# Optimization experiments

Measured on AMD Instinct MI355X. Metric: run time of the kernel, lower is better.

The kernel has to match this reference:

```python
import jax, jax.numpy as jnp
import numpy as np

B, L, D, H, FF, K = 2, 2048, 512, 16, 2048, 5
HD = D // H
EPS = 1e-5


def _ln(x, g, b):
    m = jnp.mean(x, axis=-1, keepdims=True)
    v = jnp.var(x, axis=-1, keepdims=True)
    return (x - m) / jnp.sqrt(v + EPS) * g + b


def _rope_table(seq_len, hd):
    pos = jnp.arange(seq_len, dtype=jnp.float32)
    inv = 1.0 / (10000.0 ** (jnp.arange(0, hd, 2, dtype=jnp.float32) / hd))
    ang = pos[:, None] * inv[None, :]            # [L, hd/2]
    return jnp.concatenate([jnp.cos(ang), jnp.sin(ang)], axis=-1)  # [L, hd]


def setup_inputs() -> dict:
    key = jax.random.key(0)
    ks = jax.random.split(key, 32)
    w = lambda k, shape: jax.random.normal(k, shape, jnp.float32) * 0.02
    z = lambda n: jnp.zeros((n,), jnp.float32)
    o = lambda n: jnp.ones((n,), jnp.float32)
    return {
        'src': jax.random.normal(ks[0], (B, L, D), jnp.float32),
        'Wq': w(ks[1], (D, D)), 'bq': z(D),
        'Wk': w(ks[2], (D, D)), 'bk': z(D),
        'Wv': w(ks[3], (D, D)), 'bv': z(D),
        'Wo': w(ks[4], (D, D)), 'bo': z(D),
        'ln_g': o(D), 'ln_b': z(D),
        'pw1_w': w(ks[5], (2 * D, D)), 'pw1_b': z(2 * D),
        'dw_w': w(ks[6], (D, 1, K)), 'dw_b': z(D),
        'bn_g': o(D), 'bn_b': z(D),
        'pw2_w': w(ks[7], (D, D)), 'pw2_b': z(D),
        'proj_w': w(ks[8], (L, L)), 'proj_b': z(L),
        'proj2_w': w(ks[9], (D, D)), 'proj2_b': z(D),
        'W1': w(ks[10], (FF, D)), 'b1': z(FF),
        'W2': w(ks[11], (D, FF)), 'b2': z(D),
        'n1_g': o(D), 'n1_b': z(D),
        'n2_g': o(D), 'n2_b': z(D),
    }


def reference(src, Wq, bq, Wk, bk, Wv, bv, Wo, bo, ln_g, ln_b,
              pw1_w, pw1_b, dw_w, dw_b, bn_g, bn_b, pw2_w, pw2_b,
              proj_w, proj_b, proj2_w, proj2_b, W1, b1, W2, b2,
              n1_g, n1_b, n2_g, n2_b):
    scale = HD ** -0.5
    pe = _rope_table(L, HD)
    c, s = pe[:, ::2], pe[:, 1::2]   # faithful to apply_RoPE's interleaved slicing of [cos|sin]

    def rope(x):  # x: [B,H,L,hd]
        xe, xo = x[..., ::2], x[..., 1::2]
        return jnp.concatenate([xe * c - xo * s, xe * s + xo * c], axis=-1)

    q = (src @ Wq.T + bq).reshape(B, L, H, HD).transpose(0, 2, 1, 3)
    k = (src @ Wk.T + bk).reshape(B, L, H, HD).transpose(0, 2, 1, 3)
    v = (src @ Wv.T + bv).reshape(B, L, H, HD).transpose(0, 2, 1, 3)
    q, k = rope(q), rope(k)

    slopes = jnp.asarray(2.0 ** (-(2.0 ** (-(np.log2(H) - 3.0))) * np.arange(H)), jnp.float32)
    idx = jnp.arange(L)
    dist = jnp.clip(idx[:, None] - idx[None, :], 0, None).astype(jnp.float32)
    alibi = slopes[:, None, None] * dist  # [H,L,L]

    scores = jnp.einsum('bhld,bhmd->bhlm', q, k) * scale + alibi[None]
    attn = jax.nn.softmax(scores, axis=-1)
    ctx = jnp.einsum('bhlm,bhmd->bhld', attn, v).transpose(0, 2, 1, 3).reshape(B, L, D)
    attn_out = ctx @ Wo.T + bo

    x0 = src + _ln(attn_out, n1_g, n1_b)

    # depthwise conformer conv block (stride=1, residual downsample = identity)
    x = _ln(x0, ln_g, ln_b)
    x = x @ pw1_w.T + pw1_b                      # [B,L,2D]
    a, g = x[..., :D], x[..., D:]
    x = a * jax.nn.sigmoid(g)                    # GLU
    x = x.transpose(0, 2, 1)                     # [B,D,L]
    x = jax.lax.conv_general_dilated(x, dw_w, (1,), [(K // 2, K // 2)],
                                     dimension_numbers=('NCH', 'OIH', 'NCH'),
                                     feature_group_count=D) + dw_b[None, :, None]
    x = x * (bn_g / jnp.sqrt(1.0 + EPS))[None, :, None] + bn_b[None, :, None]  # BN eval (mu=0, var=1)
    x = x * jnp.clip(x + 3.0, 0.0, 6.0) / 6.0    # hardswish
    conv = x.transpose(0, 2, 1) @ pw2_w.T + pw2_b + x0

    # seq-dim projection branch
    p = jnp.einsum('bld,ml->bmd', x0, proj_w) + proj_b[None, :, None]
    p = p @ proj2_w.T + proj2_b

    y = p + conv
    ff = jax.nn.gelu(y @ W1.T + b1, approximate=False) @ W2.T + b2
    return _ln(y + ff, n2_g, n2_b)
```

## Files before the change

kernel.cpp:

```cpp
#include <hip/hip_runtime.h>
#include <math.h>

#define B_ 2
#define L_ 2048
#define D_ 512
#define H_ 16
#define HD_ 32
#define FF_ 2048
#define BL_ 4096
#define EPS_ 1e-5f

typedef unsigned short ushort;
typedef unsigned int uint;
typedef __attribute__((ext_vector_type(8))) short bf16x8;
typedef __attribute__((ext_vector_type(4))) float f32x4;
typedef __attribute__((ext_vector_type(4))) uint u32x4;

__device__ __forceinline__ ushort bf16r(float f) {
  uint u = __float_as_uint(f);
  uint r = (u + 0x7FFFu + ((u >> 16) & 1u)) >> 16;
  return (ushort)r;
}
__device__ __forceinline__ float bf2f(uint u) { return __uint_as_float(u << 16); }

__device__ __forceinline__ float wsum(float v) {
#pragma unroll
  for (int o = 32; o; o >>= 1) v += __shfl_xor(v, o);
  return v;
}

__device__ __forceinline__ void gload16(const void* g, void* l) {
  __builtin_amdgcn_global_load_lds(
      (const __attribute__((address_space(1))) void*)g,
      (__attribute__((address_space(3))) void*)l, 16, 0, 0);
}

template <int TMv, int TNv, int EPI, int BROW, int GELU, int RES, int OUTF, int OUTB>
__global__ __launch_bounds__(256, 2) void gemm_bf_k(
    const ushort* __restrict__ A, const ushort* __restrict__ W,
    const float* __restrict__ bias, const float* __restrict__ res,
    float* __restrict__ Cf, ushort* __restrict__ Cb,
    const int M, const int N, const int Kd, const long sW, const long sC,
    const int ldC,
    const float* __restrict__ tab, ushort* __restrict__ Qb,
    ushort* __restrict__ Kb, ushort* __restrict__ Vb) {
  constexpr int MF = (TMv == 128) ? 4 : ((TNv == 128) ? 4 : 2);
  constexpr int NF = (TNv == 128) ? ((TMv == 128) ? 4 : 2) : 2;
  __shared__ __align__(16) ushort As[TMv * 64];
  __shared__ __align__(16) ushort Ws[TNv * 64];
  const int tid = threadIdx.x;
  const int wid = tid >> 6, lane = tid & 63;
  const int lane15 = lane & 15, lgrp = lane >> 4;
  const int rowoff = (TMv == 128) ? (wid >> 1) * 64
                                  : ((TNv == 64) ? (wid >> 1) * 32 : 0);
  const int wnoff = (TMv == 128) ? (wid & 1) * 64
                                 : ((TNv == 128) ? wid * 32 : (wid & 1) * 32);
  const int bm = blockIdx.y * TMv, bn = blockIdx.x * TNv;
  const int z = blockIdx.z;
  const ushort* Wz = W + (size_t)z * sW;

  f32x4 acc[MF][NF];
#pragma unroll
  for (int i = 0; i < MF; ++i)
#pragma unroll
    for (int j = 0; j < NF; ++j) acc[i][j] = (f32x4){0.f, 0.f, 0.f, 0.f};

  for (int k0 = 0; k0 < Kd; k0 += 64) {
    __syncthreads();
#pragma unroll
    for (int i = 0; i < TMv / 32; ++i) {
      const int cb = i * 256 + wid * 64;
      const int chunk = cb + lane;
      const int ml = chunk >> 3;
      const int c16 = (chunk & 7) ^ (ml & 7);
      gload16(A + (size_t)(bm + ml) * Kd + k0 + c16 * 8, &As[(size_t)cb * 8]);
    }
#pragma unroll
    for (int i = 0; i < TNv / 32; ++i) {
      const int cb = i * 256 + wid * 64;
      const int chunk = cb + lane;
      const int ml = chunk >> 3;
      const int c16 = (chunk & 7) ^ (ml & 7);
      gload16(Wz + (size_t)(bn + ml) * Kd + k0 + c16 * 8, &Ws[(size_t)cb * 8]);
    }
    __syncthreads();

    bf16x8 af[2][MF], wf[2][NF];
#pragma unroll
    for (int kk = 0; kk < 2; ++kk) {
#pragma unroll
      for (int f = 0; f < MF; ++f) {
        const int ma = rowoff + f * 16 + lane15;
        const int ca = (kk * 4 + lgrp) ^ (ma & 7);
        af[kk][f] = *(const bf16x8*)&As[ma * 64 + ca * 8];
      }
#pragma unroll
      for (int f = 0; f < NF; ++f) {
        const int nb = wnoff + f * 16 + lane15;
        const int cw = (kk * 4 + lgrp) ^ (nb & 7);
        wf[kk][f] = *(const bf16x8*)&Ws[nb * 64 + cw * 8];
      }
    }
#pragma unroll
    for (int kk = 0; kk < 2; ++kk)
#pragma unroll
      for (int fm = 0; fm < MF; ++fm)
#pragma unroll
        for (int fn = 0; fn < NF; ++fn)
          acc[fm][fn] = __builtin_amdgcn_mfma_f32_16x16x32_bf16(
              af[kk][fm], wf[kk][fn], acc[fm][fn], 0, 0, 0);
  }

#pragma unroll
  for (int fm = 0; fm < MF; ++fm) {
#pragma unroll
    for (int fn = 0; fn < NF; ++fn) {
      const int n = bn + wnoff + fn * 16 + lane15;
      float bcol = 0.f;
      if (EPI == 2) bcol = bias[(n >> 1) + (n & 1) * 512];
      else if (EPI == 1 || !BROW) bcol = bias[n];
#pragma unroll
      for (int r = 0; r < 4; ++r) {
        const int m = bm + rowoff + fm * 16 + lgrp * 4 + r;
        float val = acc[fm][fn][r];
        if (EPI == 1) {
          val += bcol;
          float p = __shfl_xor(val, 1);
          const int l = m & 2047, b = m >> 11;
          const int h = (n >> 5) & 15;
          if (n < 1024) {
            const int ch = n & 31, i2 = ch >> 1;
            const float cv = tab[l * 32 + i2], sv = tab[l * 32 + 16 + i2];
            const float o = (ch & 1) ? (p * sv + val * cv) : (val * cv - p * sv);
            const int dcol = (ch & 1) ? 16 + i2 : i2;
            if (n < 512)
              Qb[(((size_t)(b * 16 + h)) * 2048 + l) * 32 + dcol] =
                  bf16r(o * (0.1767766952966369f * 1.4426950408889634f));
            else
              Kb[(((size_t)(b * 16 + h)) * 2048 + l) * 32 + dcol] = bf16r(o);
          } else {
            Vb[(((size_t)(b * 16 + h)) * 2048 + l) * 32 + (n & 31)] = bf16r(val);
          }
        } else if (EPI == 2) {
          val += bcol;
          float p = __shfl_xor(val, 1);
          if (!(n & 1)) {
            float glu = val / (1.f + __expf(-p));
            Cb[(size_t)m * 512 + (n >> 1)] = bf16r(glu);
          }
        } else {
          val += BROW ? bias[m] : bcol;
          if (RES) val += res[(size_t)m * N + n];
          if (GELU) val = 0.5f * val * (1.f + erff(val * 0.70710678118654752f));
          const size_t o = (size_t)z * sC + (size_t)m * ldC + n;
          if (OUTF) Cf[o] = val;
          if (OUTB) Cb[o] = bf16r(val);
        }
      }
    }
  }
}

struct CvtArgs {
  const float* s[11];
  ushort* d[11];
  int n[11];
  int pm[11];
};
__global__ __launch_bounds__(256) void cvt_all_k(CvtArgs a) {
  const int seg = blockIdx.y;
  const int n = a.n[seg];
  const int i = (blockIdx.x * 256 + threadIdx.x) * 8;
  if (i >= n) return;
  const float* s = a.s[seg] + i;
  float4 x = *(const float4*)s, y = *(const float4*)(s + 4);
  bf16x8 o;
  o[0] = (short)bf16r(x.x); o[1] = (short)bf16r(x.y);
  o[2] = (short)bf16r(x.z); o[3] = (short)bf16r(x.w);
  o[4] = (short)bf16r(y.x); o[5] = (short)bf16r(y.y);
  o[6] = (short)bf16r(y.z); o[7] = (short)bf16r(y.w);
  ushort* d = a.d[seg] + i;
  const int pm = a.pm[seg];
  if (pm == 1) {
    int cc = i >> 3;
    int row = cc >> 6, off = cc & 63;
    int nrow = (row < 512) ? row * 2 : (row - 512) * 2 + 1;
    d = a.d[seg] + (((size_t)nrow << 6) + off) * 8;
  } else if (pm >= 2) {
    d = a.d[seg] + (size_t)(i >> 9) * 1024 + (i & 511) + ((pm == 3) ? 512 : 0);
  }
  *(bf16x8*)d = o;
}

__global__ void misc_k(float* __restrict__ tab, const float* __restrict__ bq,
                       const float* __restrict__ bk, const float* __restrict__ bv,
                       float* __restrict__ bqkv, const float* __restrict__ p2b,
                       const float* __restrict__ pw2b, float* __restrict__ bcat) {
  if (blockIdx.x < 128) {
    int t = blockIdx.x * 256 + threadIdx.x;
    int i = t & 15, l = t >> 4;
    float cv, sv;
    if (i < 8) {
      float inv0 = 1.0f / powf(10000.0f, (float)(2 * i) / 16.0f);
      float inv1 = 1.0f / powf(10000.0f, (float)(2 * i + 1) / 16.0f);
      cv = cosf((float)l * inv0);
      sv = cosf((float)l * inv1);
    } else {
      int ii = i - 8;
      float inv0 = 1.0f / powf(10000.0f, (float)(2 * ii) / 16.0f);
      float inv1 = 1.0f / powf(10000.0f, (float)(2 * ii + 1) / 16.0f);
      cv = sinf((float)l * inv0);
      sv = sinf((float)l * inv1);
    }
    tab[l * 32 + i] = cv;
    tab[l * 32 + 16 + i] = sv;
  } else {
    int i = threadIdx.x;
    bqkv[i] = bq[i];            bqkv[i + 256] = bq[i + 256];
    bqkv[512 + i] = bk[i];      bqkv[768 + i] = bk[i + 256];
    bqkv[1024 + i] = bv[i];     bqkv[1280 + i] = bv[i + 256];
    bcat[i] = p2b[i] + pw2b[i];
    bcat[i + 256] = p2b[i + 256] + pw2b[i + 256];
  }
}

__global__ __launch_bounds__(256) void transp_k(const float* __restrict__ x,
                                                ushort* __restrict__ xT) {
  __shared__ float t[32][33];
  const int b = blockIdx.z, l0 = blockIdx.x * 32, d0 = blockIdx.y * 32;
  const int tx = threadIdx.x & 31, ty = threadIdx.x >> 5;
#pragma unroll
  for (int i = 0; i < 4; ++i)
    t[ty + i * 8][tx] = x[((size_t)(b * L_ + l0 + ty + i * 8)) * D_ + d0 + tx];
  __syncthreads();
#pragma unroll
  for (int i = 0; i < 4; ++i)
    xT[((size_t)(b * D_ + d0 + ty + i * 8)) * L_ + l0 + tx] =
        bf16r(t[tx][ty + i * 8]);
}

__global__ __launch_bounds__(256, 4) void attn_mfma_k(const ushort* __restrict__ q,
                                                      const ushort* __restrict__ k,
                                                      const ushort* __restrict__ v,
                                                      ushort* __restrict__ ctx) {
  __shared__ __align__(16) ushort K_lds[4][130][8];
  __shared__ __align__(16) uint V_lds[32][68];
  const int tid = threadIdx.x;
  const int wid = tid >> 6, lane = tid & 63;
  const int s = lane >> 4, lr = lane & 15;
  const int bid = blockIdx.x;
  const int xcd = bid & 7, idx = bid >> 3;
  const int bh = xcd * 4 + (idx & 3);
  const int qt = idx >> 2;
  const int qb = qt * 64;
  const int h = bh & 15, bidx = bh >> 4;
  const float nslope = -exp2f(-0.5f * (float)h) * 1.4426950408889634f;
  const int qrow = qb + wid * 16 + lr;
  const float qgf = (float)qrow;
  const float cq = nslope * qgf;
  bf16x8 qa = *(const bf16x8*)&q[((size_t)bh * L_ + qrow) * HD_ + s * 8];

  float lsum = 0.f;
  f32x4 acc0 = {0.f, 0.f, 0.f, 0.f}, acc1 = {0.f, 0.f, 0.f, 0.f};
  const ushort* kg = k + (size_t)bh * L_ * HD_;
  const ushort* vg = v + (size_t)bh * L_ * HD_;
  const int vslot = (lane & 48) + ((lane >> 1) & 3) * 4 + ((lane >> 3) & 1) * 2 + (lane & 1);

  for (int t0 = 0; t0 < L_; t0 += 128) {
    __syncthreads();
#pragma unroll
    for (int pass = 0; pass < 2; ++pass) {
      int id = tid + pass * 256;
      int key = id >> 2, slot = id & 3;
      *(bf16x8*)&K_lds[slot][key][0] =
          *(const bf16x8*)&kg[(size_t)(t0 + key) * HD_ + slot * 8];
    }
    {
      const ushort* g0 = vg + (size_t)(t0 + 2 * lane) * HD_ + wid * 8;
      u32x4 va = *(const u32x4*)g0;
      u32x4 vb = *(const u32x4*)(g0 + HD_);
#pragma unroll
      for (int w = 0; w < 4; ++w) {
        V_lds[wid * 8 + 2 * w][vslot] =
            __builtin_amdgcn_perm(vb[w], va[w], 0x05040100u);
        V_lds[wid * 8 + 2 * w + 1][vslot] =
            __builtin_amdgcn_perm(vb[w], va[w], 0x07060302u);
      }
    }
    __syncthreads();

    f32x4 sc[8];
    __builtin_amdgcn_s_setprio(1);
#pragma unroll
    for (int c = 0; c < 8; ++c) {
      bf16x8 kf = *(const bf16x8*)&K_lds[s][c * 16 + lr][0];
      f32x4 zz = {0.f, 0.f, 0.f, 0.f};
      sc[c] = __builtin_amdgcn_mfma_f32_16x16x32_bf16(kf, qa, zz, 0, 0, 0);
    }
    __builtin_amdgcn_s_setprio(0);
    if (t0 + 128 <= qb) {
      const float kb0 = (float)(t0 + s * 4);
#pragma unroll
      for (int c = 0; c < 8; ++c) {
        const float kc = kb0 + (float)(c * 16);
#pragma unroll
        for (int r = 0; r < 4; ++r) {
          float p = exp2f(fmaf(nslope, kc + (float)r, sc[c][r]));
          sc[c][r] = p;
          lsum += p;
        }
      }
    } else if (t0 >= qb + 64) {
#pragma unroll
      for (int c = 0; c < 8; ++c)
#pragma unroll
        for (int r = 0; r < 4; ++r) {
          float p = exp2f(sc[c][r] + cq);
          sc[c][r] = p;
          lsum += p;
        }
    } else {
      const float kb0 = (float)(t0 + s * 4);
#pragma unroll
      for (int c = 0; c < 8; ++c) {
        const float kc = kb0 + (float)(c * 16);
#pragma unroll
        for (int r = 0; r < 4; ++r) {
          float kpos = kc + (float)r;
          float mn = fminf(kpos, qgf);
          float p = exp2f(fmaf(nslope, mn, sc[c][r]));
          sc[c][r] = p;
          lsum += p;
        }
      }
    }
#pragma unroll
    for (int t = 0; t < 4; ++t) {
      uint w0 = __builtin_amdgcn_perm(__float_as_uint(sc[2 * t][1]),
                                      __float_as_uint(sc[2 * t][0]), 0x07060302u);
      uint w1 = __builtin_amdgcn_perm(__float_as_uint(sc[2 * t][3]),
                                      __float_as_uint(sc[2 * t][2]), 0x07060302u);
      uint w2 = __builtin_amdgcn_perm(__float_as_uint(sc[2 * t + 1][1]),
                                      __float_as_uint(sc[2 * t + 1][0]), 0x07060302u);
      uint w3 = __builtin_amdgcn_perm(__float_as_uint(sc[2 * t + 1][3]),
                                      __float_as_uint(sc[2 * t + 1][2]), 0x07060302u);
      u32x4 pw = {w0, w1, w2, w3};
      bf16x8 pf = __builtin_bit_cast(bf16x8, pw);
      bf16x8 v0 = *(const bf16x8*)&V_lds[lr][t * 16 + s * 4];
      bf16x8 v1 = *(const bf16x8*)&V_lds[16 + lr][t * 16 + s * 4];
      __builtin_amdgcn_s_setprio(1);
      acc0 = __builtin_amdgcn_mfma_f32_16x16x32_bf16(pf, v0, acc0, 0, 0, 0);
      acc1 = __builtin_amdgcn_mfma_f32_16x16x32_bf16(pf, v1, acc1, 0, 0, 0);
      __builtin_amdgcn_s_setprio(0);
    }
  }
  lsum += __shfl_xor(lsum, 16);
  lsum += __shfl_xor(lsum, 32);
#pragma unroll
  for (int r = 0; r < 4; ++r) {
    float ls = __shfl(lsum, s * 4 + r, 64);
    float il = 1.f / ls;
    int qg2 = qb + wid * 16 + s * 4 + r;
    ushort* op = ctx + ((size_t)(bidx * L_ + qg2)) * D_ + h * HD_;
    op[lr] = bf16r(acc0[r] * il);
    op[16 + lr] = bf16r(acc1[r] * il);
  }
}

__global__ __launch_bounds__(64) void ln_res_ln_k(
    const float* __restrict__ x, const float* __restrict__ res,
    const float* __restrict__ g1, const float* __restrict__ b1,
    const float* __restrict__ g2, const float* __restrict__ b2,
    float* __restrict__ x0, ushort* __restrict__ xln) {
  int row = blockIdx.x, lane = threadIdx.x;
  const float* xr = x + (size_t)row * D_;
  float v[8];
  float s = 0.f, ss = 0.f;
#pragma unroll
  for (int i = 0; i < 8; ++i) {
    float t = xr[i * 64 + lane];
    v[i] = t; s += t; ss += t * t;
  }
  s = wsum(s); ss = wsum(ss);
  float mean = s * (1.f / 512.f);
  float rstd = rsqrtf(ss * (1.f / 512.f) - mean * mean + EPS_);
  float w[8];
  float s2 = 0.f, ss2 = 0.f;
#pragma unroll
  for (int i = 0; i < 8; ++i) {
    int idx = i * 64 + lane;
    float t = res[(size_t)row * D_ + idx] + (v[i] - mean) * rstd * g1[idx] + b1[idx];
    w[i] = t; s2 += t; ss2 += t * t;
  }
  s2 = wsum(s2); ss2 = wsum(ss2);
  float mean2 = s2 * (1.f / 512.f);
  float rstd2 = rsqrtf(ss2 * (1.f / 512.f) - mean2 * mean2 + EPS_);
#pragma unroll
  for (int i = 0; i < 8; ++i) {
    int idx = i * 64 + lane;
    x0[(size_t)row * D_ + idx] = w[i];
    xln[(size_t)row * D_ + idx] = bf16r((w[i] - mean2) * rstd2 * g2[idx] + b2[idx]);
  }
}

__global__ __launch_bounds__(64) void ln_k(const float* __restrict__ x,
                                           const float* __restrict__ g,
                                           const float* __restrict__ bb,
                                           float* __restrict__ out) {
  int row = blockIdx.x, lane = threadIdx.x;
  const float* xr = x + (size_t)row * D_;
  float v[8];
  float s = 0.f, ss = 0.f;
#pragma unroll
  for (int i = 0; i < 8; ++i) {
    float t = xr[i * 64 + lane];
    v[i] = t; s += t; ss += t * t;
  }
  s = wsum(s); ss = wsum(ss);
  float mean = s * (1.f / 512.f);
  float rstd = rsqrtf(ss * (1.f / 512.f) - mean * mean + EPS_);
#pragma unroll
  for (int i = 0; i < 8; ++i) {
    int idx = i * 64 + lane;
    out[(size_t)row * D_ + idx] = (v[i] - mean) * rstd * g[idx] + bb[idx];
  }
}

__global__ __launch_bounds__(256) void convbn_k(
    const ushort* __restrict__ x, const float* __restrict__ w,
    const float* __restrict__ wb, const float* __restrict__ bng,
    const float* __restrict__ bnb, ushort* __restrict__ out) {
  int t = blockIdx.x * 256 + threadIdx.x;
  int c4 = t & 127;
  int l = (t >> 7) & 2047;
  int b = t >> 18;
  int d0 = c4 * 4;
  float accv[4] = {0.f, 0.f, 0.f, 0.f};
#pragma unroll
  for (int kt = 0; kt < 5; ++kt) {
    int ls = l + kt - 2;
    if (ls >= 0 && ls < L_) {
      uint2 xv = *(const uint2*)&x[((size_t)(b * L_ + ls)) * D_ + d0];
      float pv[4] = {bf2f(xv.x & 0xffffu), bf2f(xv.x >> 16),
                     bf2f(xv.y & 0xffffu), bf2f(xv.y >> 16)};
#pragma unroll
      for (int j = 0; j < 4; ++j) accv[j] += pv[j] * w[(d0 + j) * 5 + kt];
    }
  }
  const float bscale = rsqrtf(1.0f + EPS_);
  float po[4];
#pragma unroll
  for (int j = 0; j < 4; ++j) {
    int d = d0 + j;
    float vv = accv[j] + wb[d];
    vv = vv * (bng[d] * bscale) + bnb[d];
    float hs = fminf(fmaxf(vv + 3.f, 0.f), 6.f);
    po[j] = vv * hs * (1.f / 6.f);
  }
  uint lo = (uint)bf16r(po[0]) | ((uint)bf16r(po[1]) << 16);
  uint hi = (uint)bf16r(po[2]) | ((uint)bf16r(po[3]) << 16);
  uint2 o2 = {lo, hi};
  *(uint2*)&out[((size_t)(b * L_ + l)) * 1024 + d0] = o2;
}

extern "C" void kernel_launch(void* const* d_in, const int* in_sizes, int n_in,
                              void* d_out, int out_size, void* d_ws, size_t ws_size,
                              hipStream_t stream) {
  const float* src    = (const float*)d_in[0];
  const float* Wq     = (const float*)d_in[1];
  const float* bq     = (const float*)d_in[2];
  const float* Wk     = (const float*)d_in[3];
  const float* bk     = (const float*)d_in[4];
  const float* Wv     = (const float*)d_in[5];
  const float* bv     = (const float*)d_in[6];
  const float* Wo     = (const float*)d_in[7];
  const float* bo     = (const float*)d_in[8];
  const float* ln_g   = (const float*)d_in[9];
  const float* ln_b   = (const float*)d_in[10];
  const float* pw1_w  = (const float*)d_in[11];
  const float* pw1_b  = (const float*)d_in[12];
  const float* dw_w   = (const float*)d_in[13];
  const float* dw_b   = (const float*)d_in[14];
  const float* bn_g   = (const float*)d_in[15];
  const float* bn_b   = (const float*)d_in[16];
  const float* pw2_w  = (const float*)d_in[17];
  const float* pw2_b  = (const float*)d_in[18];
  const float* proj_w = (const float*)d_in[19];
  const float* proj_b = (const float*)d_in[20];
  const float* proj2_w= (const float*)d_in[21];
  const float* proj2_b= (const float*)d_in[22];
  const float* W1     = (const float*)d_in[23];
  const float* b1     = (const float*)d_in[24];
  const float* W2     = (const float*)d_in[25];
  const float* b2     = (const float*)d_in[26];
  const float* n1_g   = (const float*)d_in[27];
  const float* n1_b   = (const float*)d_in[28];
  const float* n2_g   = (const float*)d_in[29];
  const float* n2_b   = (const float*)d_in[30];
  float* out = (float*)d_out;

  char* wsb = (char*)d_ws;
  const size_t MB1 = 1 << 20;
  ushort* wqkv = (ushort*)(wsb);
  ushort* wo_w = (ushort*)(wsb + 1536 * 1024);
  ushort* pw1w = (ushort*)(wsb + 2 * MB1);
  ushort* wcat = (ushort*)(wsb + 3 * MB1);
  ushort* pjww = (ushort*)(wsb + 4 * MB1);
  ushort* w1w  = (ushort*)(wsb + 12 * MB1);
  ushort* w2w  = (ushort*)(wsb + 14 * MB1);
  float*  bqkv = (float*)(wsb + 16 * MB1);
  float*  bcat = (float*)(wsb + 16 * MB1 + 6144);
  float*  tab  = (float*)(wsb + 16 * MB1 + 8192);
  char* A0 = wsb + 17 * MB1;
  ushort* src_bf = (ushort*)A0;
  ushort* ff_bf  = (ushort*)A0;
  float*  x0     = (float*)(A0 + 8 * MB1);
  char* B0 = A0 + 16 * MB1;
  ushort* Qb = (ushort*)B0;
  ushort* Kb = (ushort*)(B0 + 4 * MB1);
  ushort* Vb = (ushort*)(B0 + 8 * MB1);
  ushort* glu_bf = (ushort*)B0;
  ushort* xln_bf = (ushort*)(B0 + 8 * MB1);
  ushort* cat_bf = (ushort*)(B0 + 4 * MB1);
  float*  zbuf   = (float*)B0;
  char* C0 = B0 + 12 * MB1;
  ushort* ctx_bf = (ushort*)C0;
  ushort* x0T    = (ushort*)C0;
  ushort* y_bf   = (ushort*)C0;
  char* D0 = C0 + 4 * MB1;
  float* attnout = (float*)D0;
  float* y       = (float*)D0;

  dim3 blk(256);

  CvtArgs ca;
  for (int i = 0; i < 11; ++i) ca.pm[i] = 0;
  ca.s[0] = Wq;     ca.d[0] = wqkv;              ca.n[0] = 512 * 512;
  ca.s[1] = Wk;     ca.d[1] = wqkv + 512 * 512;  ca.n[1] = 512 * 512;
  ca.s[2] = Wv;     ca.d[2] = wqkv + 1024 * 512; ca.n[2] = 512 * 512;
  ca.s[3] = Wo;     ca.d[3] = wo_w;              ca.n[3] = 512 * 512;
  ca.s[4] = pw1_w;  ca.d[4] = pw1w;              ca.n[4] = 1024 * 512; ca.pm[4] = 1;
  ca.s[5] = pw2_w;  ca.d[5] = wcat;              ca.n[5] = 512 * 512;  ca.pm[5] = 3;
  ca.s[6] = proj_w; ca.d[6] = pjww;              ca.n[6] = 2048 * 2048;
  ca.s[7] = proj2_w;ca.d[7] = wcat;              ca.n[7] = 512 * 512;  ca.pm[7] = 2;
  ca.s[8] = W1;     ca.d[8] = w1w;               ca.n[8] = 2048 * 512;
  ca.s[9] = W2;     ca.d[9] = w2w;               ca.n[9] = 512 * 2048;
  ca.s[10]= src;    ca.d[10]= src_bf;            ca.n[10]= BL_ * D_;
  cvt_all_k<<<dim3(2048, 11), blk, 0, stream>>>(ca);
  misc_k<<<dim3(129), blk, 0, stream>>>(tab, bq, bk, bv, bqkv, proj2_b, pw2_b, bcat);

  gemm_bf_k<64,128,1,0,0,0,0,0><<<dim3(12, 64), blk, 0, stream>>>(
      src_bf, wqkv, bqkv, nullptr, nullptr, nullptr,
      BL_, 1536, 512, 0, 0, 1536, tab, Qb, Kb, Vb);

  attn_mfma_k<<<dim3(1024), blk, 0, stream>>>(Qb, Kb, Vb, ctx_bf);

  gemm_bf_k<64,64,0,0,0,0,1,0><<<dim3(8, 64), blk, 0, stream>>>(
      ctx_bf, wo_w, bo, nullptr, attnout, nullptr,
      BL_, 512, 512, 0, 0, 512, nullptr, nullptr, nullptr, nullptr);

  ln_res_ln_k<<<BL_, 64, 0, stream>>>(attnout, src, n1_g, n1_b, ln_g, ln_b,
                                      x0, xln_bf);

  transp_k<<<dim3(64, 16, 2), blk, 0, stream>>>(x0, x0T);

  gemm_bf_k<64,128,2,0,0,0,0,1><<<dim3(8, 64), blk, 0, stream>>>(
      xln_bf, pw1w, pw1_b, nullptr, nullptr, glu_bf,
      BL_, 1024, 512, 0, 0, 512, nullptr, nullptr, nullptr, nullptr);

  convbn_k<<<(B_ * L_ * (D_ / 4)) / 256, blk, 0, stream>>>(
      glu_bf, dw_w, dw_b, bn_g, bn_b, cat_bf + 512);

  gemm_bf_k<64,64,0,1,0,0,0,1><<<dim3(8, 32, 2), blk, 0, stream>>>(
      pjww, x0T, proj_b, nullptr, nullptr, cat_bf,
      2048, 512, 2048, (long)512 * 2048, (long)2048 * 1024, 1024,
      nullptr, nullptr, nullptr, nullptr);

  gemm_bf_k<64,64,0,0,0,1,1,1><<<dim3(8, 64), blk, 0, stream>>>(
      cat_bf, wcat, bcat, x0, y, y_bf,
      BL_, 512, 1024, 0, 0, 512, nullptr, nullptr, nullptr, nullptr);

  gemm_bf_k<128,128,0,0,1,0,0,1><<<dim3(16, 32), blk, 0, stream>>>(
      y_bf, w1w, b1, nullptr, nullptr, ff_bf,
      BL_, 2048, 512, 0, 0, 2048, nullptr, nullptr, nullptr, nullptr);

  gemm_bf_k<64,64,0,0,0,1,1,0><<<dim3(8, 64), blk, 0, stream>>>(
      ff_bf, w2w, b2, y, zbuf, nullptr,
      BL_, 512, 2048, 0, 0, 512, nullptr, nullptr, nullptr, nullptr);

  ln_k<<<BL_, 64, 0, stream>>>(zbuf, n2_g, n2_b, out);
}
```

Baseline: 241.4 us.

## Widen attention blocks to 128 queries and compute softmax denominator via MFMA

Attention blocks become 512 threads covering 128 query rows, which halves the grid and the number of times each K/V tile is staged into LDS per query. The per-lane K/V load work shrinks to match. The softmax row sum moves from scalar adds plus cross-lane shuffles to an extra MFMA against a vector of ones. That adds one MFMA per tile but removes the VALU accumulation. Larger blocks may lower occupancy, and the denominator is now built from bf16-rounded probabilities.

Measured after the change: 241.0 us. About the same (-0.2%).

```diff
diff --git a/kernel.cpp b/kernel.cpp
--- a/kernel.cpp
+++ b/kernel.cpp
@@ -239,7 +239,7 @@
         bf16r(t[tx][ty + i * 8]);
 }
 
-__global__ __launch_bounds__(256, 4) void attn_mfma_k(const ushort* __restrict__ q,
+__global__ __launch_bounds__(512, 4) void attn_mfma_k(const ushort* __restrict__ q,
                                                       const ushort* __restrict__ k,
                                                       const ushort* __restrict__ v,
                                                       ushort* __restrict__ ctx) {
@@ -252,7 +252,7 @@
   const int xcd = bid & 7, idx = bid >> 3;
   const int bh = xcd * 4 + (idx & 3);
   const int qt = idx >> 2;
-  const int qb = qt * 64;
+  const int qb = qt * 128;
   const int h = bh & 15, bidx = bh >> 4;
   const float nslope = -exp2f(-0.5f * (float)h) * 1.4426950408889634f;
   const int qrow = qb + wid * 16 + lr;
@@ -260,32 +260,31 @@
   const float cq = nslope * qgf;
   bf16x8 qa = *(const bf16x8*)&q[((size_t)bh * L_ + qrow) * HD_ + s * 8];
 
-  float lsum = 0.f;
+  bf16x8 vones;
+#pragma unroll
+  for (int i = 0; i < 8; ++i) vones[i] = (short)0x3F80;
+
   f32x4 acc0 = {0.f, 0.f, 0.f, 0.f}, acc1 = {0.f, 0.f, 0.f, 0.f};
+  f32x4 accl = {0.f, 0.f, 0.f, 0.f};
   const ushort* kg = k + (size_t)bh * L_ * HD_;
   const ushort* vg = v + (size_t)bh * L_ * HD_;
   const int vslot = (lane & 48) + ((lane >> 1) & 3) * 4 + ((lane >> 3) & 1) * 2 + (lane & 1);
 
   for (int t0 = 0; t0 < L_; t0 += 128) {
     __syncthreads();
-#pragma unroll
-    for (int pass = 0; pass < 2; ++pass) {
-      int id = tid + pass * 256;
-      int key = id >> 2, slot = id & 3;
+    {
+      int key = tid >> 2, slot = tid & 3;
       *(bf16x8*)&K_lds[slot][key][0] =
           *(const bf16x8*)&kg[(size_t)(t0 + key) * HD_ + slot * 8];
     }
     {
-      const ushort* g0 = vg + (size_t)(t0 + 2 * lane) * HD_ + wid * 8;
-      u32x4 va = *(const u32x4*)g0;
-      u32x4 vb = *(const u32x4*)(g0 + HD_);
-#pragma unroll
-      for (int w = 0; w < 4; ++w) {
-        V_lds[wid * 8 + 2 * w][vslot] =
-            __builtin_amdgcn_perm(vb[w], va[w], 0x05040100u);
-        V_lds[wid * 8 + 2 * w + 1][vslot] =
-            __builtin_amdgcn_perm(vb[w], va[w], 0x07060302u);
-      }
+      const ushort* g0 = vg + (size_t)(t0 + 2 * lane) * HD_ + wid * 4;
+      uint2 va = *(const uint2*)g0;
+      uint2 vb = *(const uint2*)(g0 + HD_);
+      V_lds[wid * 4 + 0][vslot] = __builtin_amdgcn_perm(vb.x, va.x, 0x05040100u);
+      V_lds[wid * 4 + 1][vslot] = __builtin_amdgcn_perm(vb.x, va.x, 0x07060302u);
+      V_lds[wid * 4 + 2][vslot] = __builtin_amdgcn_perm(vb.y, va.y, 0x05040100u);
+      V_lds[wid * 4 + 3][vslot] = __builtin_amdgcn_perm(vb.y, va.y, 0x07060302u);
     }
     __syncthreads();
 
@@ -298,27 +297,20 @@
       sc[c] = __builtin_amdgcn_mfma_f32_16x16x32_bf16(kf, qa, zz, 0, 0, 0);
     }
     __builtin_amdgcn_s_setprio(0);
-    if (t0 + 128 <= qb) {
+    if (t0 < qb) {
       const float kb0 = (float)(t0 + s * 4);
 #pragma unroll
       for (int c = 0; c < 8; ++c) {
         const float kc = kb0 + (float)(c * 16);
 #pragma unroll
-        for (int r = 0; r < 4; ++r) {
-          float p = exp2f(fmaf(nslope, kc + (float)r, sc[c][r]));
-          sc[c][r] = p;
-          lsum += p;
-        }
+        for (int r = 0; r < 4; ++r)
+          sc[c][r] = exp2f(fmaf(nslope, kc + (float)r, sc[c][r]));
       }
-    } else if (t0 >= qb + 64) {
+    } else if (t0 > qb) {
 #pragma unroll
       for (int c = 0; c < 8; ++c)
 #pragma unroll
-        for (int r = 0; r < 4; ++r) {
-          float p = exp2f(sc[c][r] + cq);
-          sc[c][r] = p;
-          lsum += p;
-        }
+        for (int r = 0; r < 4; ++r) sc[c][r] = exp2f(sc[c][r] + cq);
     } else {
       const float kb0 = (float)(t0 + s * 4);
 #pragma unroll
@@ -326,11 +318,8 @@
         const float kc = kb0 + (float)(c * 16);
 #pragma unroll
         for (int r = 0; r < 4; ++r) {
-          float kpos = kc + (float)r;
-          float mn = fminf(kpos, qgf);
-          float p = exp2f(fmaf(nslope, mn, sc[c][r]));
-          sc[c][r] = p;
-          lsum += p;
+          float mn = fminf(kc + (float)r, qgf);
+          sc[c][r] = exp2f(fmaf(nslope, mn, sc[c][r]));
         }
       }
     }
@@ -351,15 +340,13 @@
       __builtin_amdgcn_s_setprio(1);
       acc0 = __builtin_amdgcn_mfma_f32_16x16x32_bf16(pf, v0, acc0, 0, 0, 0);
       acc1 = __builtin_amdgcn_mfma_f32_16x16x32_bf16(pf, v1, acc1, 0, 0, 0);
+      accl = __builtin_amdgcn_mfma_f32_16x16x32_bf16(pf, vones, accl, 0, 0, 0);
       __builtin_amdgcn_s_setprio(0);
     }
   }
-  lsum += __shfl_xor(lsum, 16);
-  lsum += __shfl_xor(lsum, 32);
 #pragma unroll
   for (int r = 0; r < 4; ++r) {
-    float ls = __shfl(lsum, s * 4 + r, 64);
-    float il = 1.f / ls;
+    float il = 1.f / accl[r];
     int qg2 = qb + wid * 16 + s * 4 + r;
     ushort* op = ctx + ((size_t)(bidx * L_ + qg2)) * D_ + h * HD_;
     op[lr] = bf16r(acc0[r] * il);
@@ -553,7 +540,7 @@
       src_bf, wqkv, bqkv, nullptr, nullptr, nullptr,
       BL_, 1536, 512, 0, 0, 1536, tab, Qb, Kb, Vb);
 
-  attn_mfma_k<<<dim3(1024), blk, 0, stream>>>(Qb, Kb, Vb, ctx_bf);
+  attn_mfma_k<<<dim3(512), dim3(512), 0, stream>>>(Qb, Kb, Vb, ctx_bf);
 
   gemm_bf_k<64,64,0,0,0,0,1,0><<<dim3(8, 64), blk, 0, stream>>>(
       ctx_bf, wo_w, bo, nullptr, attnout, nullptr,
```

## Double-buffer GEMM LDS tiles and process two query tiles per attention wave

Applied to the files above, without the earlier changes.

The GEMM kernel now double-buffers its A and W tiles in LDS. It issues the next k-tile's global-to-LDS loads before computing the current one, syncing with explicit vmcnt waits and barriers. The attention kernel now has each wave handle 32 query rows, sharing each K/V LDS tile across twice the work, and the grid is halved. The softmax denominator moves from a scalar sum plus shuffles to an extra MFMA against a vector of ones. The cost is doubled LDS in the GEMM and more registers in attention, which may reduce occupancy, and the denominator is now built from bf16-rounded probabilities.

Result: slower. 319.7 us (+32.4%).

```diff
diff --git a/kernel.cpp b/kernel.cpp
--- a/kernel.cpp
+++ b/kernel.cpp
@@ -46,8 +46,9 @@
     ushort* __restrict__ Kb, ushort* __restrict__ Vb) {
   constexpr int MF = (TMv == 128) ? 4 : ((TNv == 128) ? 4 : 2);
   constexpr int NF = (TNv == 128) ? ((TMv == 128) ? 4 : 2) : 2;
-  __shared__ __align__(16) ushort As[TMv * 64];
-  __shared__ __align__(16) ushort Ws[TNv * 64];
+  constexpr int NLD = TMv / 32 + TNv / 32;
+  __shared__ __align__(16) ushort As[2][TMv * 64];
+  __shared__ __align__(16) ushort Ws[2][TNv * 64];
   const int tid = threadIdx.x;
   const int wid = tid >> 6, lane = tid & 63;
   const int lane15 = lane & 15, lgrp = lane >> 4;
@@ -58,22 +59,16 @@
   const int bm = blockIdx.y * TMv, bn = blockIdx.x * TNv;
   const int z = blockIdx.z;
   const ushort* Wz = W + (size_t)z * sW;
-
-  f32x4 acc[MF][NF];
-#pragma unroll
-  for (int i = 0; i < MF; ++i)
-#pragma unroll
-    for (int j = 0; j < NF; ++j) acc[i][j] = (f32x4){0.f, 0.f, 0.f, 0.f};
-
-  for (int k0 = 0; k0 < Kd; k0 += 64) {
-    __syncthreads();
+  const int NT = Kd >> 6;
+
+  auto STAGE = [&](ushort* dA, ushort* dW, int k0) {
 #pragma unroll
     for (int i = 0; i < TMv / 32; ++i) {
       const int cb = i * 256 + wid * 64;
       const int chunk = cb + lane;
       const int ml = chunk >> 3;
       const int c16 = (chunk & 7) ^ (ml & 7);
-      gload16(A + (size_t)(bm + ml) * Kd + k0 + c16 * 8, &As[(size_t)cb * 8]);
+      gload16(A + (size_t)(bm + ml) * Kd + k0 + c16 * 8, dA + (size_t)cb * 8);
     }
 #pragma unroll
     for (int i = 0; i < TNv / 32; ++i) {
@@ -81,9 +76,29 @@
       const int chunk = cb + lane;
       const int ml = chunk >> 3;
       const int c16 = (chunk & 7) ^ (ml & 7);
-      gload16(Wz + (size_t)(bn + ml) * Kd + k0 + c16 * 8, &Ws[(size_t)cb * 8]);
-    }
-    __syncthreads();
+      gload16(Wz + (size_t)(bn + ml) * Kd + k0 + c16 * 8, dW + (size_t)cb * 8);
+    }
+  };
+
+  f32x4 acc[MF][NF];
+#pragma unroll
+  for (int i = 0; i < MF; ++i)
+#pragma unroll
+    for (int j = 0; j < NF; ++j) acc[i][j] = (f32x4){0.f, 0.f, 0.f, 0.f};
+
+  STAGE(&As[0][0], &Ws[0][0], 0);
+
+  int cur = 0;
+  for (int t = 0; t < NT; ++t) {
+    const int nxt = cur ^ 1;
+    if (t + 1 < NT) {
+      STAGE(&As[nxt][0], &Ws[nxt][0], (t + 1) << 6);
+      asm volatile("s_waitcnt vmcnt(%0)" ::"n"(NLD) : "memory");
+    } else {
+      asm volatile("s_waitcnt vmcnt(0)" ::: "memory");
+    }
+    __builtin_amdgcn_s_barrier();
+    __builtin_amdgcn_sched_barrier(0);
 
     bf16x8 af[2][MF], wf[2][NF];
 #pragma unroll
@@ -92,13 +107,13 @@
       for (int f = 0; f < MF; ++f) {
         const int ma = rowoff + f * 16 + lane15;
         const int ca = (kk * 4 + lgrp) ^ (ma & 7);
-        af[kk][f] = *(const bf16x8*)&As[ma * 64 + ca * 8];
+        af[kk][f] = *(const bf16x8*)&As[cur][ma * 64 + ca * 8];
       }
 #pragma unroll
       for (int f = 0; f < NF; ++f) {
         const int nb = wnoff + f * 16 + lane15;
         const int cw = (kk * 4 + lgrp) ^ (nb & 7);
-        wf[kk][f] = *(const bf16x8*)&Ws[nb * 64 + cw * 8];
+        wf[kk][f] = *(const bf16x8*)&Ws[cur][nb * 64 + cw * 8];
       }
     }
 #pragma unroll
@@ -109,6 +124,10 @@
         for (int fn = 0; fn < NF; ++fn)
           acc[fm][fn] = __builtin_amdgcn_mfma_f32_16x16x32_bf16(
               af[kk][fm], wf[kk][fn], acc[fm][fn], 0, 0, 0);
+
+    asm volatile("" ::: "memory");
+    __builtin_amdgcn_s_barrier();
+    cur = nxt;
   }
 
 #pragma unroll
@@ -252,16 +271,23 @@
   const int xcd = bid & 7, idx = bid >> 3;
   const int bh = xcd * 4 + (idx & 3);
   const int qt = idx >> 2;
-  const int qb = qt * 64;
+  const int qb = qt * 128;
   const int h = bh & 15, bidx = bh >> 4;
   const float nslope = -exp2f(-0.5f * (float)h) * 1.4426950408889634f;
-  const int qrow = qb + wid * 16 + lr;
-  const float qgf = (float)qrow;
-  const float cq = nslope * qgf;
-  bf16x8 qa = *(const bf16x8*)&q[((size_t)bh * L_ + qrow) * HD_ + s * 8];
-
-  float lsum = 0.f;
-  f32x4 acc0 = {0.f, 0.f, 0.f, 0.f}, acc1 = {0.f, 0.f, 0.f, 0.f};
+  const int qrowA = qb + wid * 32 + lr;
+  const int qrowB = qrowA + 16;
+  const float qgfA = (float)qrowA, qgfB = (float)qrowB;
+  const float cqA = nslope * qgfA, cqB = nslope * qgfB;
+  bf16x8 qa0 = *(const bf16x8*)&q[((size_t)bh * L_ + qrowA) * HD_ + s * 8];
+  bf16x8 qa1 = *(const bf16x8*)&q[((size_t)bh * L_ + qrowB) * HD_ + s * 8];
+
+  bf16x8 vones;
+#pragma unroll
+  for (int i = 0; i < 8; ++i) vones[i] = (short)0x3F80;
+
+  f32x4 accA0 = {0.f, 0.f, 0.f, 0.f}, accA1 = {0.f, 0.f, 0.f, 0.f};
+  f32x4 accB0 = {0.f, 0.f, 0.f, 0.f}, accB1 = {0.f, 0.f, 0.f, 0.f};
+  f32x4 acclA = {0.f, 0.f, 0.f, 0.f}, acclB = {0.f, 0.f, 0.f, 0.f};
   const ushort* kg = k + (size_t)bh * L_ * HD_;
   const ushort* vg = v + (size_t)bh * L_ * HD_;
   const int vslot = (lane & 48) + ((lane >> 1) & 3) * 4 + ((lane >> 3) & 1) * 2 + (lane & 1);
@@ -289,35 +315,35 @@
     }
     __syncthreads();
 
-    f32x4 sc[8];
+    f32x4 sa[8], sb[8];
     __builtin_amdgcn_s_setprio(1);
 #pragma unroll
     for (int c = 0; c < 8; ++c) {
       bf16x8 kf = *(const bf16x8*)&K_lds[s][c * 16 + lr][0];
       f32x4 zz = {0.f, 0.f, 0.f, 0.f};
-      sc[c] = __builtin_amdgcn_mfma_f32_16x16x32_bf16(kf, qa, zz, 0, 0, 0);
+      sa[c] = __builtin_amdgcn_mfma_f32_16x16x32_bf16(kf, qa0, zz, 0, 0, 0);
+      sb[c] = __builtin_amdgcn_mfma_f32_16x16x32_bf16(kf, qa1, zz, 0, 0, 0);
     }
     __builtin_amdgcn_s_setprio(0);
-    if (t0 + 128 <= qb) {
+    if (t0 < qb) {
       const float kb0 = (float)(t0 + s * 4);
 #pragma unroll
       for (int c = 0; c < 8; ++c) {
         const float kc = kb0 + (float)(c * 16);
 #pragma unroll
         for (int r = 0; r < 4; ++r) {
-          float p = exp2f(fmaf(nslope, kc + (float)r, sc[c][r]));
-          sc[c][r] = p;
-          lsum += p;
+          float w = fmaf(nslope, kc + (float)r, 0.f);
+          sa[c][r] = exp2f(sa[c][r] + w);
+          sb[c][r] = exp2f(sb[c][r] + w);
         }
       }
-    } else if (t0 >= qb + 64) {
+    } else if (t0 > qb) {
 #pragma unroll
       for (int c = 0; c < 8; ++c)
 #pragma unroll
         for (int r = 0; r < 4; ++r) {
-          float p = exp2f(sc[c][r] + cq);
-          sc[c][r] = p;
-          lsum += p;
+          sa[c][r] = exp2f(sa[c][r] + cqA);
+          sb[c][r] = exp2f(sb[c][r] + cqB);
         }
     } else {
       const float kb0 = (float)(t0 + s * 4);
@@ -327,43 +353,57 @@
 #pragma unroll
         for (int r = 0; r < 4; ++r) {
           float kpos = kc + (float)r;
-          float mn = fminf(kpos, qgf);
-          float p = exp2f(fmaf(nslope, mn, sc[c][r]));
-          sc[c][r] = p;
-          lsum += p;
+          sa[c][r] = exp2f(fmaf(nslope, fminf(kpos, qgfA), sa[c][r]));
+          sb[c][r] = exp2f(fmaf(nslope, fminf(kpos, qgfB), sb[c][r]));
         }
       }
     }
 #pragma unroll
     for (int t = 0; t < 4; ++t) {
-      uint w0 = __builtin_amdgcn_perm(__float_as_uint(sc[2 * t][1]),
-                                      __float_as_uint(sc[2 * t][0]), 0x07060302u);
-      uint w1 = __builtin_amdgcn_perm(__float_as_uint(sc[2 * t][3]),
-                                      __float_as_uint(sc[2 * t][2]), 0x07060302u);
-      uint w2 = __builtin_amdgcn_perm(__float_as_uint(sc[2 * t + 1][1]),
-                                      __float_as_uint(sc[2 * t + 1][0]), 0x07060302u);
-      uint w3 = __builtin_amdgcn_perm(__float_as_uint(sc[2 * t + 1][3]),
-                                      __float_as_uint(sc[2 * t + 1][2]), 0x07060302u);
-      u32x4 pw = {w0, w1, w2, w3};
-      bf16x8 pf = __builtin_bit_cast(bf16x8, pw);
+      uint a0 = __builtin_amdgcn_perm(__float_as_uint(sa[2 * t][1]),
+                                      __float_as_uint(sa[2 * t][0]), 0x07060302u);
+      uint a1 = __builtin_amdgcn_perm(__float_as_uint(sa[2 * t][3]),
+                                      __float_as_uint(sa[2 * t][2]), 0x07060302u);
+      uint a2 = __builtin_amdgcn_perm(__float_as_uint(sa[2 * t + 1][1]),
+                                      __float_as_uint(sa[2 * t + 1][0]), 0x07060302u);
+      uint a3 = __builtin_amdgcn_perm(__float_as_uint(sa[2 * t + 1][3]),
+                                      __float_as_uint(sa[2 * t + 1][2]), 0x07060302u);
+      uint b0 = __builtin_amdgcn_perm(__float_as_uint(sb[2 * t][1]),
+                                      __float_as_uint(sb[2 * t][0]), 0x07060302u);
+      uint b1 = __builtin_amdgcn_perm(__float_as_uint(sb[2 * t][3]),
+                                      __float_as_uint(sb[2 * t][2]), 0x07060302u);
+      uint b2 = __builtin_amdgcn_perm(__float_as_uint(sb[2 * t + 1][1]),
+                                      __float_as_uint(sb[2 * t + 1][0]), 0x07060302u);
+      uint b3 = __builtin_amdgcn_perm(__float_as_uint(sb[2 * t + 1][3]),
+                                      __float_as_uint(sb[2 * t + 1][2]), 0x07060302u);
+      u32x4 pwa = {a0, a1, a2, a3};
+      u32x4 pwb = {b0, b1, b2, b3};
+      bf16x8 pfA = __builtin_bit_cast(bf16x8, pwa);
+      bf16x8 pfB = __builtin_bit_cast(bf16x8, pwb);
       bf16x8 v0 = *(const bf16x8*)&V_lds[lr][t * 16 + s * 4];
       bf16x8 v1 = *(const bf16x8*)&V_lds[16 + lr][t * 16 + s * 4];
       __builtin_amdgcn_s_setprio(1);
-      acc0 = __builtin_amdgcn_mfma_f32_16x16x32_bf16(pf, v0, acc0, 0, 0, 0);
-      acc1 = __builtin_amdgcn_mfma_f32_16x16x32_bf16(pf, v1, acc1, 0, 0, 0);
+      accA0 = __builtin_amdgcn_mfma_f32_16x16x32_bf16(pfA, v0, accA0, 0, 0, 0);
+      accA1 = __builtin_amdgcn_mfma_f32_16x16x32_bf16(pfA, v1, accA1, 0, 0, 0);
+      acclA = __builtin_amdgcn_mfma_f32_16x16x32_bf16(pfA, vones, acclA, 0, 0, 0);
+      accB0 = __builtin_amdgcn_mfma_f32_16x16x32_bf16(pfB, v0, accB0, 0, 0, 0);
+      accB1 = __builtin_amdgcn_mfma_f32_16x16x32_bf16(pfB, v1, accB1, 0, 0, 0);
+      acclB = __builtin_amdgcn_mfma_f32_16x16x32_bf16(pfB, vones, acclB, 0, 0, 0);
       __builtin_amdgcn_s_setprio(0);
     }
   }
-  lsum += __shfl_xor(lsum, 16);
-  lsum += __shfl_xor(lsum, 32);
 #pragma unroll
   for (int r = 0; r < 4; ++r) {
-    float ls = __shfl(lsum, s * 4 + r, 64);
-    float il = 1.f / ls;
-    int qg2 = qb + wid * 16 + s * 4 + r;
-    ushort* op = ctx + ((size_t)(bidx * L_ + qg2)) * D_ + h * HD_;
-    op[lr] = bf16r(acc0[r] * il);
-    op[16 + lr] = bf16r(acc1[r] * il);
+    int qgA = qb + wid * 32 + s * 4 + r;
+    float ilA = 1.f / acclA[r];
+    ushort* opA = ctx + ((size_t)(bidx * L_ + qgA)) * D_ + h * HD_;
+    opA[lr] = bf16r(accA0[r] * ilA);
+    opA[16 + lr] = bf16r(accA1[r] * ilA);
+    int qgB = qgA + 16;
+    float ilB = 1.f / acclB[r];
+    ushort* opB = ctx + ((size_t)(bidx * L_ + qgB)) * D_ + h * HD_;
+    opB[lr] = bf16r(accB0[r] * ilB);
+    opB[16 + lr] = bf16r(accB1[r] * ilB);
   }
 }
 
@@ -553,7 +593,7 @@
       src_bf, wqkv, bqkv, nullptr, nullptr, nullptr,
       BL_, 1536, 512, 0, 0, 1536, tab, Qb, Kb, Vb);
 
-  attn_mfma_k<<<dim3(1024), blk, 0, stream>>>(Qb, Kb, Vb, ctx_bf);
+  attn_mfma_k<<<dim3(512), blk, 0, stream>>>(Qb, Kb, Vb, ctx_bf);
 
   gemm_bf_k<64,64,0,0,0,0,1,0><<<dim3(8, 64), blk, 0, stream>>>(
       ctx_bf, wo_w, bo, nullptr, attnout, nullptr,
```
